# Performance work log

Hardware: AMD Instinct MI355X
Metric: run time of the kernel (lower is better)

## Reference

```python
import jax, jax.numpy as jnp
import numpy as np
import math

B, S, D, H = 1, 4096, 1024, 16
DH = D // H  # head_dim = 64
NEG = -10000.0  # matches torch masked-fill value in source (not -inf)


def setup_inputs() -> dict:
    key = jax.random.key(0)
    ks = jax.random.split(key, 5)
    scale = 0.02
    return {
        "x": jax.random.normal(ks[0], (B, S, D), dtype=jnp.float32),
        "Wqkv_w": jax.random.normal(ks[1], (3 * D, D), dtype=jnp.float32) * scale,
        "Wqkv_b": jax.random.normal(ks[2], (3 * D,), dtype=jnp.float32) * scale,
        "out_w": jax.random.normal(ks[3], (D, D), dtype=jnp.float32) * scale,
        "out_b": jax.random.normal(ks[4], (D,), dtype=jnp.float32) * scale,
    }


def reference(x, Wqkv_w, Wqkv_b, out_w, out_b):
    # QKV projection: (B,S,D) @ (D,3D) + b -> (B,S,3,H,DH)
    qkv = jnp.einsum('bsd,ed->bse', x, Wqkv_w) + Wqkv_b
    qkv = qkv.reshape(B, S, 3, H, DH)
    q, k, v = qkv[:, :, 0], qkv[:, :, 1], qkv[:, :, 2]  # each (B,S,H,DH)
    softmax_scale = 1.0 / math.sqrt(DH)
    # scores: (B,H,T,S)
    scores = jnp.einsum('bthd,bshd->bhts', q, k * softmax_scale)
    # causal additive mask with -10000 above diagonal (faithful to source)
    causal_mask = jnp.triu(jnp.full((S, S), NEG, dtype=scores.dtype), k=1)
    scores = scores + causal_mask
    attention = jax.nn.softmax(scores, axis=-1)
    context = jnp.einsum('bhts,bshd->bthd', attention, v)  # (B,T,H,DH)
    context = context.reshape(B, S, D)
    out = jnp.einsum('bsd,ed->bse', context, out_w) + out_b
    return out
```

## Files before the change

### kernel.cpp

```cpp
#include <hip/hip_runtime.h>
#include <hip/hip_bf16.h>

using f32x4  = __attribute__((ext_vector_type(4))) float;
using f32x16 = __attribute__((ext_vector_type(16))) float;
using bf16x8 = __attribute__((ext_vector_type(8))) __bf16;
using u16x8  = __attribute__((ext_vector_type(8))) unsigned short;
using u32x4  = __attribute__((ext_vector_type(4))) unsigned int;

#define DEV __device__ __forceinline__

constexpr int S_  = 4096;
constexpr int D_  = 1024;
constexpr int KD  = 1024;

constexpr size_t XB_OFF   = 0;
constexpr size_t WQKV_OFF = 8388608;
constexpr size_t WOUT_OFF = 14680064;
constexpr size_t QB_OFF   = 16777216;
constexpr size_t KB_OFF   = 25165824;
constexpr size_t VT_OFF   = 33554432;
constexpr size_t CTX_OFF  = 41943040;

DEV unsigned short f2bf(float f) {
  __hip_bfloat16 h = __float2bfloat16(f);
  return __builtin_bit_cast(unsigned short, h);
}

DEV void gl_lds16(const void* g, void* l) {
  __builtin_amdgcn_global_load_lds(
      (const __attribute__((address_space(1))) void*)g,
      (__attribute__((address_space(3))) void*)l, 16, 0, 0);
}

DEV f32x4 mfma16(bf16x8 a, bf16x8 b, f32x4 c) {
  return __builtin_amdgcn_mfma_f32_16x16x32_bf16(a, b, c, 0, 0, 0);
}
DEV f32x16 mfma32(bf16x8 a, bf16x8 b, f32x16 c) {
  return __builtin_amdgcn_mfma_f32_32x32x16_bf16(a, b, c, 0, 0, 0);
}
DEV unsigned cvtpk(float lo, float hi) {
  unsigned r;
  asm("v_cvt_pk_bf16_f32 %0, %1, %2" : "=v"(r) : "v"(lo), "v"(hi));
  return r;
}
DEV float exp2_fast(float x) {
  float r;
  asm("v_exp_f32 %0, %1" : "=v"(r) : "v"(x));
  return r;
}
DEV void pl32(unsigned& a, unsigned& b) {
  asm("v_permlane32_swap_b32 %0, %1" : "+v"(a), "+v"(b));
}
DEV float xhalf_add(float x) {
  float y;
  asm("v_mov_b32 %0, %1" : "=v"(y) : "v"(x));
  unsigned a = __builtin_bit_cast(unsigned, x), b = __builtin_bit_cast(unsigned, y);
  pl32(a, b);
  return __builtin_bit_cast(float, a) + __builtin_bit_cast(float, b);
}

__global__ void cvt_all_k(const float* __restrict__ x,
                          const float* __restrict__ wq,
                          const float* __restrict__ wo,
                          unsigned short* __restrict__ xb,
                          unsigned short* __restrict__ wqb,
                          unsigned short* __restrict__ wob) {
  for (int u = blockIdx.x * 256 + threadIdx.x; u < 1048576; u += 2048 * 256) {
    const float* s; unsigned short* d; int off;
    if (u < 524288)      { s = x;  d = xb;  off = u; }
    else if (u < 917504) { s = wq; d = wqb; off = u - 524288; }
    else                 { s = wo; d = wob; off = u - 917504; }
    const float4* s4 = (const float4*)s;
    float4 a = s4[2 * off], b = s4[2 * off + 1];
    u16x8 o;
    o[0] = f2bf(a.x); o[1] = f2bf(a.y); o[2] = f2bf(a.z); o[3] = f2bf(a.w);
    o[4] = f2bf(b.x); o[5] = f2bf(b.y); o[6] = f2bf(b.z); o[7] = f2bf(b.w);
    ((u16x8*)d)[off] = o;
  }
}

__global__ __launch_bounds__(256)
void gemm_qkv_k(const unsigned short* __restrict__ A,
                const unsigned short* __restrict__ Bt,
                const float* __restrict__ bias,
                unsigned short* __restrict__ qb,
                unsigned short* __restrict__ kb,
                unsigned short* __restrict__ vt) {
  __shared__ unsigned short As[2][4096];
  __shared__ unsigned short Bs[2][4096];
  const int t = threadIdx.x;
  const int w = t >> 6, l = t & 63;
  const int lr = l & 15, lg = l >> 4, lk = lg * 8;
  const int m0 = blockIdx.y * 128, n0 = blockIdx.x * 128;
  const int wm = (w >> 1) * 64, wn = (w & 1) * 64;

  f32x4 acc[4][4] = {};

  const int srow = t >> 2;
  const int scolb = (t & 3) << 4;
  const char* Ag = (const char*)A + (size_t)(m0 + srow) * (KD * 2) + scolb;
  const char* Bg = (const char*)Bt + (size_t)(n0 + srow) * (KD * 2) + scolb;

  auto stage = [&](int buf, int kt) {
    const char* ak = Ag + kt * 64;
    const char* bk = Bg + kt * 64;
    char* AsB = (char*)&As[buf][0];
    char* BsB = (char*)&Bs[buf][0];
    gl_lds16(ak,                 AsB + t * 16);
    gl_lds16(ak + 64 * (KD * 2), AsB + 4096 + t * 16);
    gl_lds16(bk,                 BsB + t * 16);
    gl_lds16(bk + 64 * (KD * 2), BsB + 4096 + t * 16);
  };

  stage(0, 0);
  for (int kt = 0; kt < KD / 32; ++kt) {
    __syncthreads();
    if (kt + 1 < KD / 32) stage((kt + 1) & 1, kt + 1);
    const int buf = kt & 1;

    bf16x8 a[4], b[4];
#pragma unroll
    for (int mi = 0; mi < 4; ++mi)
      a[mi] = *(const bf16x8*)&As[buf][(wm + mi * 16 + lr) * 32 + lk];
#pragma unroll
    for (int ni = 0; ni < 4; ++ni)
      b[ni] = *(const bf16x8*)&Bs[buf][(wn + ni * 16 + lr) * 32 + lk];
#pragma unroll
    for (int mi = 0; mi < 4; ++mi)
#pragma unroll
      for (int ni = 0; ni < 4; ++ni)
        acc[mi][ni] = mfma16(a[mi], b[ni], acc[mi][ni]);
  }

  const int r0 = lg * 4;
  const int which = n0 >> 10;
  const float kscale = 0.125f * 1.44269504088896f;
#pragma unroll
  for (int mi = 0; mi < 4; ++mi) {
    const int sbase = m0 + wm + mi * 16 + r0;
#pragma unroll
    for (int ni = 0; ni < 4; ++ni) {
      const int e = n0 + wn + ni * 16 + lr;
      const float bv = bias[e];
      const int h = (e & 1023) >> 6, dd = e & 63;
#pragma unroll
      for (int r = 0; r < 4; ++r) {
        const float v = acc[mi][ni][r] + bv;
        const int sr = sbase + r;
        if (which == 0)      qb[((size_t)(h * S_ + sr)) * 64 + dd] = f2bf(v);
        else if (which == 1) kb[((size_t)(h * S_ + sr)) * 64 + dd] = f2bf(v * kscale);
        else                 vt[((size_t)(h * 64 + dd)) * S_ + sr] = f2bf(v);
      }
    }
  }
}

__global__ __launch_bounds__(256)
void gemm_proj_k(const unsigned short* __restrict__ A,
                 const unsigned short* __restrict__ Bt,
                 const float* __restrict__ bias,
                 float* __restrict__ outf) {
  __shared__ unsigned short As[2][4096];
  __shared__ unsigned short Bs[2][2048];
  const int t = threadIdx.x;
  const int w = t >> 6, l = t & 63;
  const int lr = l & 15, lg = l >> 4, lk = lg * 8;
  const int m0 = blockIdx.y * 128, n0 = blockIdx.x * 64;
  const int wm = (w >> 1) * 64, wn = (w & 1) * 32;

  f32x4 acc[4][2] = {};

  const int srow = t >> 2;
  const int scolb = (t & 3) << 4;
  const char* Ag = (const char*)A + (size_t)(m0 + srow) * (KD * 2) + scolb;
  const char* Bg = (const char*)Bt + (size_t)(n0 + (t >> 2)) * (KD * 2) + scolb;

  auto stage = [&](int buf, int kt) {
    const char* ak = Ag + kt * 64;
    char* AsB = (char*)&As[buf][0];
    gl_lds16(ak,                 AsB + t * 16);
    gl_lds16(ak + 64 * (KD * 2), AsB + 4096 + t * 16);
    gl_lds16(Bg + kt * 64, (char*)&Bs[buf][0] + t * 16);
  };

  stage(0, 0);
  for (int kt = 0; kt < KD / 32; ++kt) {
    __syncthreads();
    if (kt + 1 < KD / 32) stage((kt + 1) & 1, kt + 1);
    const int buf = kt & 1;

    bf16x8 a[4], b[2];
#pragma unroll
    for (int mi = 0; mi < 4; ++mi)
      a[mi] = *(const bf16x8*)&As[buf][(wm + mi * 16 + lr) * 32 + lk];
#pragma unroll
    for (int ni = 0; ni < 2; ++ni)
      b[ni] = *(const bf16x8*)&Bs[buf][(wn + ni * 16 + lr) * 32 + lk];
#pragma unroll
    for (int mi = 0; mi < 4; ++mi)
#pragma unroll
      for (int ni = 0; ni < 2; ++ni)
        acc[mi][ni] = mfma16(a[mi], b[ni], acc[mi][ni]);
  }

  const int r0 = lg * 4;
#pragma unroll
  for (int mi = 0; mi < 4; ++mi) {
    const int sbase = m0 + wm + mi * 16 + r0;
#pragma unroll
    for (int ni = 0; ni < 2; ++ni) {
      const int e = n0 + wn + ni * 16 + lr;
      const float bv = bias[e];
#pragma unroll
      for (int r = 0; r < 4; ++r)
        outf[(size_t)(sbase + r) * D_ + e] = acc[mi][ni][r] + bv;
    }
  }
}

__global__ __launch_bounds__(512, 2)
void attn_k(const unsigned short* __restrict__ Qb,
            const unsigned short* __restrict__ Kb,
            const unsigned short* __restrict__ Vt,
            unsigned short* __restrict__ ctx) {
  __shared__ char smem[65536];

  const int t = threadIdx.x;
  const int w8 = t >> 6;
  const int g  = w8 >> 2;
  const int w  = w8 & 3;
  const int l = t & 63, lq = l & 31, hi = l >> 5;
  const int b = blockIdx.x + (blockIdx.y << 4);
  const int h = ((b & 7) << 1) | ((b >> 3) & 1);
  const int pairIdx = b >> 4;

  const int sg = t >> 8;
  const int ts = t & 255;
  const int srow = ts >> 3;
  const int ssw  = ((ts & 7) << 4) ^ ((srow & 7) << 4);
  const char* Kg0 = (const char*)Kb + (size_t)(h * S_) * 128;
  const char* Vg0 = (const char*)Vt + (size_t)(h * 64) * (size_t)(S_ * 2);

  for (int task = 0; task < 2; ++task) {
    const int bi = task == 0 ? (31 - pairIdx) : pairIdx;
    const int q0 = bi * 128;
    const int qrow = q0 + w * 32 + lq;
    const int qwmin = q0 + w * 32, qwmax = qwmin + 31;
    const int niter = bi + 1;

    const unsigned short* Qr = Qb + ((size_t)(h * S_ + qrow)) * 64;
    bf16x8 qf[4];
#pragma unroll
    for (int d0 = 0; d0 < 4; ++d0)
      qf[d0] = *(const bf16x8*)(Qr + d0 * 16 + hi * 8);

    f32x16 cacc[2] = {};
    float lsum = 0.f;

    auto stage = [&](int buf, int tl) {
      const int kv0 = tl * 64;
      char* kd = smem + sg * 16384 + buf * 8192;
      const char* Kg = Kg0 + (size_t)kv0 * 128;
      gl_lds16(Kg + (size_t)srow * 128 + ssw,        kd + ts * 16);
      gl_lds16(Kg + (size_t)(32 + srow) * 128 + ssw, kd + 4096 + ts * 16);
      char* vd = smem + 32768 + sg * 16384 + buf * 8192;
      const char* Vg = Vg0 + (size_t)kv0 * 2;
      gl_lds16(Vg + (size_t)srow * (S_ * 2) + ssw,        vd + ts * 16);
      gl_lds16(Vg + (size_t)(32 + srow) * (S_ * 2) + ssw, vd + 4096 + ts * 16);
    };

    int cur = 0;
    stage(0, sg * niter);

    for (int it = 0; it < niter; ++it) {
      __syncthreads();
      if (it + 1 < niter) stage(cur ^ 1, it + 1 + sg * niter);
      const char* Kt = smem + g * 16384 + cur * 8192;
      const char* Vl = smem + 32768 + g * 16384 + cur * 8192;
      const int tl = it + g * niter;

      if (tl * 64 + 63 <= qwmin) {
        f32x16 st0, st1;
#pragma unroll
        for (int r = 0; r < 16; ++r) { st0[r] = -8.0f; st1[r] = -8.0f; }
        const char* kb0 = Kt + lq * 128;
        const char* kb1 = Kt + (32 + lq) * 128;
        const int ksw = (lq & 7) << 4;
        __builtin_amdgcn_s_setprio(1);
#pragma unroll
        for (int d0 = 0; d0 < 4; ++d0) {
          bf16x8 kf0 = *(const bf16x8*)(kb0 + ((d0 * 32 + hi * 16) ^ ksw));
          bf16x8 kf1 = *(const bf16x8*)(kb1 + ((d0 * 32 + hi * 16) ^ ksw));
          st0 = mfma32(kf0, qf[d0], st0);
          st1 = mfma32(kf1, qf[d0], st1);
        }
        __builtin_amdgcn_s_setprio(0);

#pragma unroll
        for (int r = 0; r < 16; ++r) { st0[r] = exp2_fast(st0[r]); st1[r] = exp2_fast(st1[r]); }
        float a0 = (st0[0] + st0[1]) + (st0[2] + st0[3]);
        float a1 = (st0[4] + st0[5]) + (st0[6] + st0[7]);
        float a2 = (st0[8] + st0[9]) + (st0[10] + st0[11]);
        float a3 = (st0[12] + st0[13]) + (st0[14] + st0[15]);
        float b0 = (st1[0] + st1[1]) + (st1[2] + st1[3]);
        float b1 = (st1[4] + st1[5]) + (st1[6] + st1[7]);
        float b2 = (st1[8] + st1[9]) + (st1[10] + st1[11]);
        float b3 = (st1[12] + st1[13]) + (st1[14] + st1[15]);
        lsum += xhalf_add(((a0 + a1) + (a2 + a3)) + ((b0 + b1) + (b2 + b3)));

        unsigned x0 = cvtpk(st0[0], st0[1]),   x1 = cvtpk(st0[2], st0[3]);
        unsigned y0 = cvtpk(st0[4], st0[5]),   y1 = cvtpk(st0[6], st0[7]);
        pl32(x0, y0); pl32(x1, y1);
        u32x4 f00 = {x0, x1, y0, y1};
        bf16x8 pf00 = __builtin_bit_cast(bf16x8, f00);
        unsigned x2 = cvtpk(st0[8], st0[9]),   x3 = cvtpk(st0[10], st0[11]);
        unsigned y2 = cvtpk(st0[12], st0[13]), y3 = cvtpk(st0[14], st0[15]);
        pl32(x2, y2); pl32(x3, y3);
        u32x4 f01 = {x2, x3, y2, y3};
        bf16x8 pf01 = __builtin_bit_cast(bf16x8, f01);
        unsigned u0 = cvtpk(st1[0], st1[1]),   u1 = cvtpk(st1[2], st1[3]);
        unsigned v0w = cvtpk(st1[4], st1[5]),  v1w = cvtpk(st1[6], st1[7]);
        pl32(u0, v0w); pl32(u1, v1w);
        u32x4 f10 = {u0, u1, v0w, v1w};
        bf16x8 pf10 = __builtin_bit_cast(bf16x8, f10);
        unsigned u2 = cvtpk(st1[8], st1[9]),   u3 = cvtpk(st1[10], st1[11]);
        unsigned v2w = cvtpk(st1[12], st1[13]), v3w = cvtpk(st1[14], st1[15]);
        pl32(u2, v2w); pl32(u3, v3w);
        u32x4 f11 = {u2, u3, v2w, v3w};
        bf16x8 pf11 = __builtin_bit_cast(bf16x8, f11);

        __builtin_amdgcn_s_setprio(1);
#pragma unroll
        for (int db = 0; db < 2; ++db) {
          const int dr = db * 32 + lq;
          const char* vbase = Vl + dr * 128;
          const int vsw = (dr & 7) << 4;
          bf16x8 va = *(const bf16x8*)(vbase + ((hi * 16) ^ vsw));
          bf16x8 vb = *(const bf16x8*)(vbase + ((32 + hi * 16) ^ vsw));
          bf16x8 vc = *(const bf16x8*)(vbase + ((64 + hi * 16) ^ vsw));
          bf16x8 vd = *(const bf16x8*)(vbase + ((96 + hi * 16) ^ vsw));
          cacc[db] = mfma32(va, pf00, cacc[db]);
          cacc[db] = mfma32(vb, pf01, cacc[db]);
          cacc[db] = mfma32(vc, pf10, cacc[db]);
          cacc[db] = mfma32(vd, pf11, cacc[db]);
        }
        __builtin_amdgcn_s_setprio(0);
      } else {
#pragma unroll
        for (int kvh = 0; kvh < 2; ++kvh) {
          const int kv0s = tl * 64 + kvh * 32;
          if (kv0s > qwmax) continue;

          f32x16 st;
#pragma unroll
          for (int r = 0; r < 16; ++r) st[r] = -8.0f;
          const int kr = kvh * 32 + lq;
          const char* kbase = Kt + kr * 128;
          const int ksw = (kr & 7) << 4;
#pragma unroll
          for (int d0 = 0; d0 < 4; ++d0) {
            bf16x8 kf = *(const bf16x8*)(kbase + ((d0 * 32 + hi * 16) ^ ksw));
            st = mfma32(kf, qf[d0], st);
          }

          if (kv0s + 31 > qwmin) {
#pragma unroll
            for (int r = 0; r < 16; ++r) {
              const int kvg = kv0s + (r & 3) + 8 * (r >> 2) + 4 * hi;
              if (kvg > qrow) st[r] = -INFINITY;
            }
          }

#pragma unroll
          for (int r = 0; r < 16; ++r) st[r] = exp2_fast(st[r]);
          float a0 = (st[0] + st[1]) + (st[2] + st[3]);
          float a1 = (st[4] + st[5]) + (st[6] + st[7]);
          float a2 = (st[8] + st[9]) + (st[10] + st[11]);
          float a3 = (st[12] + st[13]) + (st[14] + st[15]);
          lsum += xhalf_add((a0 + a1) + (a2 + a3));

          unsigned x0 = cvtpk(st[0], st[1]),   x1 = cvtpk(st[2], st[3]);
          unsigned y0 = cvtpk(st[4], st[5]),   y1 = cvtpk(st[6], st[7]);
          pl32(x0, y0); pl32(x1, y1);
          u32x4 f0 = {x0, x1, y0, y1};
          bf16x8 pf0 = __builtin_bit_cast(bf16x8, f0);
          unsigned x2 = cvtpk(st[8], st[9]),   x3 = cvtpk(st[10], st[11]);
          unsigned y2 = cvtpk(st[12], st[13]), y3 = cvtpk(st[14], st[15]);
          pl32(x2, y2); pl32(x3, y3);
          u32x4 f1 = {x2, x3, y2, y3};
          bf16x8 pf1 = __builtin_bit_cast(bf16x8, f1);

#pragma unroll
          for (int db = 0; db < 2; ++db) {
            const int dr = db * 32 + lq;
            const char* vbase = Vl + dr * 128;
            const int vsw = (dr & 7) << 4;
            bf16x8 v0 = *(const bf16x8*)(vbase + ((kvh * 64 + hi * 16) ^ vsw));
            bf16x8 v1 = *(const bf16x8*)(vbase + ((kvh * 64 + 32 + hi * 16) ^ vsw));
            cacc[db] = mfma32(v0, pf0, cacc[db]);
            cacc[db] = mfma32(v1, pf1, cacc[db]);
          }
        }
      }
      cur ^= 1;
    }

    __syncthreads();
    float* slot = (float*)smem + (size_t)(w * 64 + l) * 36;
    if (g == 1) {
      slot[0] = lsum;
#pragma unroll
      for (int j = 0; j < 16; ++j) { slot[1 + j] = cacc[0][j]; slot[17 + j] = cacc[1][j]; }
    }
    __syncthreads();
    if (g == 0) {
      const float inv = 1.0f / (lsum + slot[0]);
      unsigned short* base = ctx + (size_t)qrow * D_ + h * 64;
#pragma unroll
      for (int db = 0; db < 2; ++db)
#pragma unroll
        for (int r = 0; r < 16; r += 2) {
          const float o0 = (cacc[db][r]     + slot[1 + db * 16 + r])     * inv;
          const float o1 = (cacc[db][r + 1] + slot[1 + db * 16 + r + 1]) * inv;
          const unsigned wv = cvtpk(o0, o1);
          const int d = (r & 3) + 8 * (r >> 2) + 4 * hi + 32 * db;
          *(unsigned*)(base + d) = wv;
        }
    }
    __syncthreads();
  }
}

extern "C" void kernel_launch(void* const* d_in, const int* in_sizes, int n_in,
                              void* d_out, int out_size, void* d_ws, size_t ws_size,
                              hipStream_t stream) {
  const float* x      = (const float*)d_in[0];
  const float* Wqkv_w = (const float*)d_in[1];
  const float* Wqkv_b = (const float*)d_in[2];
  const float* out_w  = (const float*)d_in[3];
  const float* out_b  = (const float*)d_in[4];
  float* out = (float*)d_out;
  char* ws = (char*)d_ws;

  unsigned short* xb    = (unsigned short*)(ws + XB_OFF);
  unsigned short* wqkvb = (unsigned short*)(ws + WQKV_OFF);
  unsigned short* woutb = (unsigned short*)(ws + WOUT_OFF);
  unsigned short* Qb    = (unsigned short*)(ws + QB_OFF);
  unsigned short* Kb    = (unsigned short*)(ws + KB_OFF);
  unsigned short* Vt    = (unsigned short*)(ws + VT_OFF);
  unsigned short* ctx   = (unsigned short*)(ws + CTX_OFF);

  cvt_all_k<<<2048, 256, 0, stream>>>(x, Wqkv_w, out_w, xb, wqkvb, woutb);

  gemm_qkv_k<<<dim3(24, 32), 256, 0, stream>>>(xb, wqkvb, Wqkv_b, Qb, Kb, Vt);

  attn_k<<<dim3(16, 16), 512, 0, stream>>>(Qb, Kb, Vt, ctx);

  gemm_proj_k<<<dim3(16, 32), 256, 0, stream>>>(ctx, woutb, out_b, out);
}
```

Measured before the change: 131.4 us.

## Process 128-row KV tiles per iteration in the causal attention kernel

Doubles the K/V tile staged in LDS per loop iteration from 64 to 128 keys. This halves the number of iterations and block barriers per query tile. The KV range is now split between the two wave groups as contiguous halves rather than interleaved tiles. The V layout moves to 256-byte rows with a new swizzle. Shared memory doubles to 128 KB per block, which likely stops two 512-thread blocks from fitting on a CU and lowers occupancy.

```diff
diff --git a/kernel.cpp b/kernel.cpp
--- a/kernel.cpp
+++ b/kernel.cpp
@@ -223,7 +223,7 @@
             const unsigned short* __restrict__ Kb,
             const unsigned short* __restrict__ Vt,
             unsigned short* __restrict__ ctx) {
-  __shared__ char smem[65536];
+  __shared__ char smem[131072];
 
   const int t = threadIdx.x;
   const int w8 = t >> 6;
@@ -236,8 +236,10 @@
 
   const int sg = t >> 8;
   const int ts = t & 255;
-  const int srow = ts >> 3;
-  const int ssw  = ((ts & 7) << 4) ^ ((srow & 7) << 4);
+  const int srow  = ts >> 3;
+  const int ssw   = ((ts & 7) << 4) ^ ((srow & 7) << 4);
+  const int srowV = ts >> 4;
+  const int ssv   = ((ts & 15) << 4) ^ ((srowV & 7) << 4);
   const char* Kg0 = (const char*)Kb + (size_t)(h * S_) * 128;
   const char* Vg0 = (const char*)Vt + (size_t)(h * 64) * (size_t)(S_ * 2);
 
@@ -246,7 +248,10 @@
     const int q0 = bi * 128;
     const int qrow = q0 + w * 32 + lq;
     const int qwmin = q0 + w * 32, qwmax = qwmin + 31;
-    const int niter = bi + 1;
+    const int niter  = (bi + 2) >> 1;
+    const int sgbase = sg == 0 ? 0 : (bi + 1) * 64;
+    const int gbase  = g  == 0 ? 0 : (bi + 1) * 64;
+    const int kvend  = g == 0 ? (bi + 1) * 64 : S_;
 
     const unsigned short* Qr = Qb + ((size_t)(h * S_ + qrow)) * 64;
     bf16x8 qf[4];
@@ -257,106 +262,110 @@
     f32x16 cacc[2] = {};
     float lsum = 0.f;
 
-    auto stage = [&](int buf, int tl) {
-      const int kv0 = tl * 64;
-      char* kd = smem + sg * 16384 + buf * 8192;
+    auto stage = [&](int buf, int tt) {
+      const int kv0 = sgbase + tt * 128;
+      char* kd = smem + sg * 32768 + buf * 16384;
       const char* Kg = Kg0 + (size_t)kv0 * 128;
-      gl_lds16(Kg + (size_t)srow * 128 + ssw,        kd + ts * 16);
-      gl_lds16(Kg + (size_t)(32 + srow) * 128 + ssw, kd + 4096 + ts * 16);
-      char* vd = smem + 32768 + sg * 16384 + buf * 8192;
+#pragma unroll
+      for (int c = 0; c < 4; ++c)
+        gl_lds16(Kg + (size_t)(srow + c * 32) * 128 + ssw, kd + c * 4096 + ts * 16);
+      char* vd = smem + 65536 + sg * 32768 + buf * 16384;
       const char* Vg = Vg0 + (size_t)kv0 * 2;
-      gl_lds16(Vg + (size_t)srow * (S_ * 2) + ssw,        vd + ts * 16);
-      gl_lds16(Vg + (size_t)(32 + srow) * (S_ * 2) + ssw, vd + 4096 + ts * 16);
+#pragma unroll
+      for (int c = 0; c < 4; ++c)
+        gl_lds16(Vg + (size_t)(srowV + c * 16) * (S_ * 2) + ssv, vd + c * 4096 + ts * 16);
     };
 
     int cur = 0;
-    stage(0, sg * niter);
+    stage(0, 0);
 
     for (int it = 0; it < niter; ++it) {
       __syncthreads();
-      if (it + 1 < niter) stage(cur ^ 1, it + 1 + sg * niter);
-      const char* Kt = smem + g * 16384 + cur * 8192;
-      const char* Vl = smem + 32768 + g * 16384 + cur * 8192;
-      const int tl = it + g * niter;
-
-      if (tl * 64 + 63 <= qwmin) {
-        f32x16 st0, st1;
-#pragma unroll
-        for (int r = 0; r < 16; ++r) { st0[r] = -8.0f; st1[r] = -8.0f; }
-        const char* kb0 = Kt + lq * 128;
-        const char* kb1 = Kt + (32 + lq) * 128;
-        const int ksw = (lq & 7) << 4;
-        __builtin_amdgcn_s_setprio(1);
-#pragma unroll
-        for (int d0 = 0; d0 < 4; ++d0) {
-          bf16x8 kf0 = *(const bf16x8*)(kb0 + ((d0 * 32 + hi * 16) ^ ksw));
-          bf16x8 kf1 = *(const bf16x8*)(kb1 + ((d0 * 32 + hi * 16) ^ ksw));
-          st0 = mfma32(kf0, qf[d0], st0);
-          st1 = mfma32(kf1, qf[d0], st1);
+      if (it + 1 < niter) stage(cur ^ 1, it + 1);
+      const char* Kt = smem + g * 32768 + cur * 16384;
+      const char* Vl = smem + 65536 + g * 32768 + cur * 16384;
+      const int tk0 = gbase + it * 128;
+
+      if (tk0 + 127 <= qwmin && tk0 + 128 <= kvend) {
+#pragma unroll
+        for (int hf = 0; hf < 2; ++hf) {
+          f32x16 st0, st1;
+#pragma unroll
+          for (int r = 0; r < 16; ++r) { st0[r] = -8.0f; st1[r] = -8.0f; }
+          const char* kb0 = Kt + (hf * 64 + lq) * 128;
+          const char* kb1 = Kt + (hf * 64 + 32 + lq) * 128;
+          const int ksw = (lq & 7) << 4;
+          __builtin_amdgcn_s_setprio(1);
+#pragma unroll
+          for (int d0 = 0; d0 < 4; ++d0) {
+            bf16x8 kf0 = *(const bf16x8*)(kb0 + ((d0 * 32 + hi * 16) ^ ksw));
+            bf16x8 kf1 = *(const bf16x8*)(kb1 + ((d0 * 32 + hi * 16) ^ ksw));
+            st0 = mfma32(kf0, qf[d0], st0);
+            st1 = mfma32(kf1, qf[d0], st1);
+          }
+          __builtin_amdgcn_s_setprio(0);
+
+#pragma unroll
+          for (int r = 0; r < 16; ++r) { st0[r] = exp2_fast(st0[r]); st1[r] = exp2_fast(st1[r]); }
+          float a0 = (st0[0] + st0[1]) + (st0[2] + st0[3]);
+          float a1 = (st0[4] + st0[5]) + (st0[6] + st0[7]);
+          float a2 = (st0[8] + st0[9]) + (st0[10] + st0[11]);
+          float a3 = (st0[12] + st0[13]) + (st0[14] + st0[15]);
+          float b0 = (st1[0] + st1[1]) + (st1[2] + st1[3]);
+          float b1 = (st1[4] + st1[5]) + (st1[6] + st1[7]);
+          float b2 = (st1[8] + st1[9]) + (st1[10] + st1[11]);
+          float b3 = (st1[12] + st1[13]) + (st1[14] + st1[15]);
+          lsum += xhalf_add(((a0 + a1) + (a2 + a3)) + ((b0 + b1) + (b2 + b3)));
+
+          unsigned x0 = cvtpk(st0[0], st0[1]),   x1 = cvtpk(st0[2], st0[3]);
+          unsigned y0 = cvtpk(st0[4], st0[5]),   y1 = cvtpk(st0[6], st0[7]);
+          pl32(x0, y0); pl32(x1, y1);
+          u32x4 f00 = {x0, x1, y0, y1};
+          bf16x8 pf00 = __builtin_bit_cast(bf16x8, f00);
+          unsigned x2 = cvtpk(st0[8], st0[9]),   x3 = cvtpk(st0[10], st0[11]);
+          unsigned y2 = cvtpk(st0[12], st0[13]), y3 = cvtpk(st0[14], st0[15]);
+          pl32(x2, y2); pl32(x3, y3);
+          u32x4 f01 = {x2, x3, y2, y3};
+          bf16x8 pf01 = __builtin_bit_cast(bf16x8, f01);
+          unsigned u0 = cvtpk(st1[0], st1[1]),    u1 = cvtpk(st1[2], st1[3]);
+          unsigned v0w = cvtpk(st1[4], st1[5]),   v1w = cvtpk(st1[6], st1[7]);
+          pl32(u0, v0w); pl32(u1, v1w);
+          u32x4 f10 = {u0, u1, v0w, v1w};
+          bf16x8 pf10 = __builtin_bit_cast(bf16x8, f10);
+          unsigned u2 = cvtpk(st1[8], st1[9]),    u3 = cvtpk(st1[10], st1[11]);
+          unsigned v2w = cvtpk(st1[12], st1[13]), v3w = cvtpk(st1[14], st1[15]);
+          pl32(u2, v2w); pl32(u3, v3w);
+          u32x4 f11 = {u2, u3, v2w, v3w};
+          bf16x8 pf11 = __builtin_bit_cast(bf16x8, f11);
+
+          __builtin_amdgcn_s_setprio(1);
+#pragma unroll
+          for (int db = 0; db < 2; ++db) {
+            const int dr = db * 32 + lq;
+            const char* vbase = Vl + dr * 256;
+            const int vsw = (dr & 7) << 4;
+            bf16x8 va = *(const bf16x8*)(vbase + ((hf * 128 + hi * 16) ^ vsw));
+            bf16x8 vb = *(const bf16x8*)(vbase + ((hf * 128 + 32 + hi * 16) ^ vsw));
+            bf16x8 vc = *(const bf16x8*)(vbase + ((hf * 128 + 64 + hi * 16) ^ vsw));
+            bf16x8 vd = *(const bf16x8*)(vbase + ((hf * 128 + 96 + hi * 16) ^ vsw));
+            cacc[db] = mfma32(va, pf00, cacc[db]);
+            cacc[db] = mfma32(vb, pf01, cacc[db]);
+            cacc[db] = mfma32(vc, pf10, cacc[db]);
+            cacc[db] = mfma32(vd, pf11, cacc[db]);
+          }
+          __builtin_amdgcn_s_setprio(0);
         }
-        __builtin_amdgcn_s_setprio(0);
-
-#pragma unroll
-        for (int r = 0; r < 16; ++r) { st0[r] = exp2_fast(st0[r]); st1[r] = exp2_fast(st1[r]); }
-        float a0 = (st0[0] + st0[1]) + (st0[2] + st0[3]);
-        float a1 = (st0[4] + st0[5]) + (st0[6] + st0[7]);
-        float a2 = (st0[8] + st0[9]) + (st0[10] + st0[11]);
-        float a3 = (st0[12] + st0[13]) + (st0[14] + st0[15]);
-        float b0 = (st1[0] + st1[1]) + (st1[2] + st1[3]);
-        float b1 = (st1[4] + st1[5]) + (st1[6] + st1[7]);
-        float b2 = (st1[8] + st1[9]) + (st1[10] + st1[11]);
-        float b3 = (st1[12] + st1[13]) + (st1[14] + st1[15]);
-        lsum += xhalf_add(((a0 + a1) + (a2 + a3)) + ((b0 + b1) + (b2 + b3)));
-
-        unsigned x0 = cvtpk(st0[0], st0[1]),   x1 = cvtpk(st0[2], st0[3]);
-        unsigned y0 = cvtpk(st0[4], st0[5]),   y1 = cvtpk(st0[6], st0[7]);
-        pl32(x0, y0); pl32(x1, y1);
-        u32x4 f00 = {x0, x1, y0, y1};
-        bf16x8 pf00 = __builtin_bit_cast(bf16x8, f00);
-        unsigned x2 = cvtpk(st0[8], st0[9]),   x3 = cvtpk(st0[10], st0[11]);
-        unsigned y2 = cvtpk(st0[12], st0[13]), y3 = cvtpk(st0[14], st0[15]);
-        pl32(x2, y2); pl32(x3, y3);
-        u32x4 f01 = {x2, x3, y2, y3};
-        bf16x8 pf01 = __builtin_bit_cast(bf16x8, f01);
-        unsigned u0 = cvtpk(st1[0], st1[1]),   u1 = cvtpk(st1[2], st1[3]);
-        unsigned v0w = cvtpk(st1[4], st1[5]),  v1w = cvtpk(st1[6], st1[7]);
-        pl32(u0, v0w); pl32(u1, v1w);
-        u32x4 f10 = {u0, u1, v0w, v1w};
-        bf16x8 pf10 = __builtin_bit_cast(bf16x8, f10);
-        unsigned u2 = cvtpk(st1[8], st1[9]),   u3 = cvtpk(st1[10], st1[11]);
-        unsigned v2w = cvtpk(st1[12], st1[13]), v3w = cvtpk(st1[14], st1[15]);
-        pl32(u2, v2w); pl32(u3, v3w);
-        u32x4 f11 = {u2, u3, v2w, v3w};
-        bf16x8 pf11 = __builtin_bit_cast(bf16x8, f11);
-
-        __builtin_amdgcn_s_setprio(1);
-#pragma unroll
-        for (int db = 0; db < 2; ++db) {
-          const int dr = db * 32 + lq;
-          const char* vbase = Vl + dr * 128;
-          const int vsw = (dr & 7) << 4;
-          bf16x8 va = *(const bf16x8*)(vbase + ((hi * 16) ^ vsw));
-          bf16x8 vb = *(const bf16x8*)(vbase + ((32 + hi * 16) ^ vsw));
-          bf16x8 vc = *(const bf16x8*)(vbase + ((64 + hi * 16) ^ vsw));
-          bf16x8 vd = *(const bf16x8*)(vbase + ((96 + hi * 16) ^ vsw));
-          cacc[db] = mfma32(va, pf00, cacc[db]);
-          cacc[db] = mfma32(vb, pf01, cacc[db]);
-          cacc[db] = mfma32(vc, pf10, cacc[db]);
-          cacc[db] = mfma32(vd, pf11, cacc[db]);
-        }
-        __builtin_amdgcn_s_setprio(0);
       } else {
 #pragma unroll
-        for (int kvh = 0; kvh < 2; ++kvh) {
-          const int kv0s = tl * 64 + kvh * 32;
-          if (kv0s > qwmax) continue;
+        for (int s = 0; s < 4; ++s) {
+          const int kv0s = tk0 + s * 32;
+          if (kv0s >= kvend || kv0s > qwmax) continue;
 
           f32x16 st;
 #pragma unroll
           for (int r = 0; r < 16; ++r) st[r] = -8.0f;
-          const int kr = kvh * 32 + lq;
-          const char* kbase = Kt + kr * 128;
-          const int ksw = (kr & 7) << 4;
+          const char* kbase = Kt + (s * 32 + lq) * 128;
+          const int ksw = (lq & 7) << 4;
 #pragma unroll
           for (int d0 = 0; d0 < 4; ++d0) {
             bf16x8 kf = *(const bf16x8*)(kbase + ((d0 * 32 + hi * 16) ^ ksw));
@@ -393,10 +402,10 @@
 #pragma unroll
           for (int db = 0; db < 2; ++db) {
             const int dr = db * 32 + lq;
-            const char* vbase = Vl + dr * 128;
+            const char* vbase = Vl + dr * 256;
             const int vsw = (dr & 7) << 4;
-            bf16x8 v0 = *(const bf16x8*)(vbase + ((kvh * 64 + hi * 16) ^ vsw));
-            bf16x8 v1 = *(const bf16x8*)(vbase + ((kvh * 64 + 32 + hi * 16) ^ vsw));
+            bf16x8 v0 = *(const bf16x8*)(vbase + ((s * 64 + hi * 16) ^ vsw));
+            bf16x8 v1 = *(const bf16x8*)(vbase + ((s * 64 + 32 + hi * 16) ^ vsw));
             cacc[db] = mfma32(v0, pf0, cacc[db]);
             cacc[db] = mfma32(v1, pf1, cacc[db]);
           }
```

Measured after the change: 130.4 us. Within noise of the previous version (-0.8%).

## Halve attention query tile to 64 rows, using 256-thread blocks and twice the blocks

Applied to the files above, without the earlier changes.

The causal attention kernel now processes 64 query rows per block with 4 waves instead of 128 rows with 8 waves, and launches twice as many blocks. The KV tiles of a query block are split between two wave groups, with a guard for an odd tile count. Each thread now issues four async loads per staged K and V tile instead of two. The aim is finer load balancing and more scheduling freedom across CUs, at the cost of streaming K and V from global memory twice as often per query row.

```diff
diff --git a/kernel.cpp b/kernel.cpp
--- a/kernel.cpp
+++ b/kernel.cpp
@@ -218,7 +218,7 @@
   }
 }
 
-__global__ __launch_bounds__(512, 2)
+__global__ __launch_bounds__(256, 2)
 void attn_k(const unsigned short* __restrict__ Qb,
             const unsigned short* __restrict__ Kb,
             const unsigned short* __restrict__ Vt,
@@ -226,27 +226,29 @@
   __shared__ char smem[65536];
 
   const int t = threadIdx.x;
-  const int w8 = t >> 6;
-  const int g  = w8 >> 2;
-  const int w  = w8 & 3;
+  const int w4 = t >> 6;
+  const int g  = w4 >> 1;
+  const int w  = w4 & 1;
   const int l = t & 63, lq = l & 31, hi = l >> 5;
-  const int b = blockIdx.x + (blockIdx.y << 4);
+  const int b = blockIdx.x + (blockIdx.y << 5);
   const int h = ((b & 7) << 1) | ((b >> 3) & 1);
   const int pairIdx = b >> 4;
 
-  const int sg = t >> 8;
-  const int ts = t & 255;
+  const int sg = t >> 7;
+  const int ts = t & 127;
   const int srow = ts >> 3;
   const int ssw  = ((ts & 7) << 4) ^ ((srow & 7) << 4);
   const char* Kg0 = (const char*)Kb + (size_t)(h * S_) * 128;
   const char* Vg0 = (const char*)Vt + (size_t)(h * 64) * (size_t)(S_ * 2);
 
   for (int task = 0; task < 2; ++task) {
-    const int bi = task == 0 ? (31 - pairIdx) : pairIdx;
-    const int q0 = bi * 128;
+    const int bi = task == 0 ? (63 - pairIdx) : pairIdx;
+    const int q0 = bi * 64;
     const int qrow = q0 + w * 32 + lq;
     const int qwmin = q0 + w * 32, qwmax = qwmin + 31;
-    const int niter = bi + 1;
+    const int ntiles = bi + 1;
+    const int niter  = (ntiles + 1) >> 1;
+    const int mycnt  = sg == 0 ? niter : (ntiles - niter);
 
     const unsigned short* Qr = Qb + ((size_t)(h * S_ + qrow)) * 64;
     bf16x8 qf[4];
@@ -257,148 +259,152 @@
     f32x16 cacc[2] = {};
     float lsum = 0.f;
 
-    auto stage = [&](int buf, int tl) {
-      const int kv0 = tl * 64;
+    auto stage = [&](int buf, int idx) {
+      const int kv0 = ((sg ? niter : 0) + idx) * 64;
       char* kd = smem + sg * 16384 + buf * 8192;
       const char* Kg = Kg0 + (size_t)kv0 * 128;
-      gl_lds16(Kg + (size_t)srow * 128 + ssw,        kd + ts * 16);
-      gl_lds16(Kg + (size_t)(32 + srow) * 128 + ssw, kd + 4096 + ts * 16);
+#pragma unroll
+      for (int c = 0; c < 4; ++c)
+        gl_lds16(Kg + (size_t)(srow + c * 16) * 128 + ssw, kd + c * 2048 + ts * 16);
       char* vd = smem + 32768 + sg * 16384 + buf * 8192;
       const char* Vg = Vg0 + (size_t)kv0 * 2;
-      gl_lds16(Vg + (size_t)srow * (S_ * 2) + ssw,        vd + ts * 16);
-      gl_lds16(Vg + (size_t)(32 + srow) * (S_ * 2) + ssw, vd + 4096 + ts * 16);
+#pragma unroll
+      for (int c = 0; c < 4; ++c)
+        gl_lds16(Vg + (size_t)(srow + c * 16) * (S_ * 2) + ssw, vd + c * 2048 + ts * 16);
     };
 
     int cur = 0;
-    stage(0, sg * niter);
+    if (mycnt > 0) stage(0, 0);
 
     for (int it = 0; it < niter; ++it) {
       __syncthreads();
-      if (it + 1 < niter) stage(cur ^ 1, it + 1 + sg * niter);
-      const char* Kt = smem + g * 16384 + cur * 8192;
-      const char* Vl = smem + 32768 + g * 16384 + cur * 8192;
-      const int tl = it + g * niter;
-
-      if (tl * 64 + 63 <= qwmin) {
-        f32x16 st0, st1;
-#pragma unroll
-        for (int r = 0; r < 16; ++r) { st0[r] = -8.0f; st1[r] = -8.0f; }
-        const char* kb0 = Kt + lq * 128;
-        const char* kb1 = Kt + (32 + lq) * 128;
-        const int ksw = (lq & 7) << 4;
-        __builtin_amdgcn_s_setprio(1);
-#pragma unroll
-        for (int d0 = 0; d0 < 4; ++d0) {
-          bf16x8 kf0 = *(const bf16x8*)(kb0 + ((d0 * 32 + hi * 16) ^ ksw));
-          bf16x8 kf1 = *(const bf16x8*)(kb1 + ((d0 * 32 + hi * 16) ^ ksw));
-          st0 = mfma32(kf0, qf[d0], st0);
-          st1 = mfma32(kf1, qf[d0], st1);
-        }
-        __builtin_amdgcn_s_setprio(0);
-
-#pragma unroll
-        for (int r = 0; r < 16; ++r) { st0[r] = exp2_fast(st0[r]); st1[r] = exp2_fast(st1[r]); }
-        float a0 = (st0[0] + st0[1]) + (st0[2] + st0[3]);
-        float a1 = (st0[4] + st0[5]) + (st0[6] + st0[7]);
-        float a2 = (st0[8] + st0[9]) + (st0[10] + st0[11]);
-        float a3 = (st0[12] + st0[13]) + (st0[14] + st0[15]);
-        float b0 = (st1[0] + st1[1]) + (st1[2] + st1[3]);
-        float b1 = (st1[4] + st1[5]) + (st1[6] + st1[7]);
-        float b2 = (st1[8] + st1[9]) + (st1[10] + st1[11]);
-        float b3 = (st1[12] + st1[13]) + (st1[14] + st1[15]);
-        lsum += xhalf_add(((a0 + a1) + (a2 + a3)) + ((b0 + b1) + (b2 + b3)));
-
-        unsigned x0 = cvtpk(st0[0], st0[1]),   x1 = cvtpk(st0[2], st0[3]);
-        unsigned y0 = cvtpk(st0[4], st0[5]),   y1 = cvtpk(st0[6], st0[7]);
-        pl32(x0, y0); pl32(x1, y1);
-        u32x4 f00 = {x0, x1, y0, y1};
-        bf16x8 pf00 = __builtin_bit_cast(bf16x8, f00);
-        unsigned x2 = cvtpk(st0[8], st0[9]),   x3 = cvtpk(st0[10], st0[11]);
-        unsigned y2 = cvtpk(st0[12], st0[13]), y3 = cvtpk(st0[14], st0[15]);
-        pl32(x2, y2); pl32(x3, y3);
-        u32x4 f01 = {x2, x3, y2, y3};
-        bf16x8 pf01 = __builtin_bit_cast(bf16x8, f01);
-        unsigned u0 = cvtpk(st1[0], st1[1]),   u1 = cvtpk(st1[2], st1[3]);
-        unsigned v0w = cvtpk(st1[4], st1[5]),  v1w = cvtpk(st1[6], st1[7]);
-        pl32(u0, v0w); pl32(u1, v1w);
-        u32x4 f10 = {u0, u1, v0w, v1w};
-        bf16x8 pf10 = __builtin_bit_cast(bf16x8, f10);
-        unsigned u2 = cvtpk(st1[8], st1[9]),   u3 = cvtpk(st1[10], st1[11]);
-        unsigned v2w = cvtpk(st1[12], st1[13]), v3w = cvtpk(st1[14], st1[15]);
-        pl32(u2, v2w); pl32(u3, v3w);
-        u32x4 f11 = {u2, u3, v2w, v3w};
-        bf16x8 pf11 = __builtin_bit_cast(bf16x8, f11);
-
-        __builtin_amdgcn_s_setprio(1);
-#pragma unroll
-        for (int db = 0; db < 2; ++db) {
-          const int dr = db * 32 + lq;
-          const char* vbase = Vl + dr * 128;
-          const int vsw = (dr & 7) << 4;
-          bf16x8 va = *(const bf16x8*)(vbase + ((hi * 16) ^ vsw));
-          bf16x8 vb = *(const bf16x8*)(vbase + ((32 + hi * 16) ^ vsw));
-          bf16x8 vc = *(const bf16x8*)(vbase + ((64 + hi * 16) ^ vsw));
-          bf16x8 vd = *(const bf16x8*)(vbase + ((96 + hi * 16) ^ vsw));
-          cacc[db] = mfma32(va, pf00, cacc[db]);
-          cacc[db] = mfma32(vb, pf01, cacc[db]);
-          cacc[db] = mfma32(vc, pf10, cacc[db]);
-          cacc[db] = mfma32(vd, pf11, cacc[db]);
-        }
-        __builtin_amdgcn_s_setprio(0);
-      } else {
-#pragma unroll
-        for (int kvh = 0; kvh < 2; ++kvh) {
-          const int kv0s = tl * 64 + kvh * 32;
-          if (kv0s > qwmax) continue;
-
-          f32x16 st;
-#pragma unroll
-          for (int r = 0; r < 16; ++r) st[r] = -8.0f;
-          const int kr = kvh * 32 + lq;
-          const char* kbase = Kt + kr * 128;
-          const int ksw = (kr & 7) << 4;
+      if (it + 1 < mycnt) stage(cur ^ 1, it + 1);
+      const int tl = (g ? niter : 0) + it;
+      if (tl < ntiles) {
+        const char* Kt = smem + g * 16384 + cur * 8192;
+        const char* Vl = smem + 32768 + g * 16384 + cur * 8192;
+
+        if (tl * 64 + 63 <= qwmin) {
+          f32x16 st0, st1;
+#pragma unroll
+          for (int r = 0; r < 16; ++r) { st0[r] = -8.0f; st1[r] = -8.0f; }
+          const char* kb0 = Kt + lq * 128;
+          const char* kb1 = Kt + (32 + lq) * 128;
+          const int ksw = (lq & 7) << 4;
+          __builtin_amdgcn_s_setprio(1);
 #pragma unroll
           for (int d0 = 0; d0 < 4; ++d0) {
-            bf16x8 kf = *(const bf16x8*)(kbase + ((d0 * 32 + hi * 16) ^ ksw));
-            st = mfma32(kf, qf[d0], st);
+            bf16x8 kf0 = *(const bf16x8*)(kb0 + ((d0 * 32 + hi * 16) ^ ksw));
+            bf16x8 kf1 = *(const bf16x8*)(kb1 + ((d0 * 32 + hi * 16) ^ ksw));
+            st0 = mfma32(kf0, qf[d0], st0);
+            st1 = mfma32(kf1, qf[d0], st1);
           }
-
-          if (kv0s + 31 > qwmin) {
-#pragma unroll
-            for (int r = 0; r < 16; ++r) {
-              const int kvg = kv0s + (r & 3) + 8 * (r >> 2) + 4 * hi;
-              if (kvg > qrow) st[r] = -INFINITY;
-            }
-          }
-
-#pragma unroll
-          for (int r = 0; r < 16; ++r) st[r] = exp2_fast(st[r]);
-          float a0 = (st[0] + st[1]) + (st[2] + st[3]);
-          float a1 = (st[4] + st[5]) + (st[6] + st[7]);
-          float a2 = (st[8] + st[9]) + (st[10] + st[11]);
-          float a3 = (st[12] + st[13]) + (st[14] + st[15]);
-          lsum += xhalf_add((a0 + a1) + (a2 + a3));
-
-          unsigned x0 = cvtpk(st[0], st[1]),   x1 = cvtpk(st[2], st[3]);
-          unsigned y0 = cvtpk(st[4], st[5]),   y1 = cvtpk(st[6], st[7]);
+          __builtin_amdgcn_s_setprio(0);
+
+#pragma unroll
+          for (int r = 0; r < 16; ++r) { st0[r] = exp2_fast(st0[r]); st1[r] = exp2_fast(st1[r]); }
+          float a0 = (st0[0] + st0[1]) + (st0[2] + st0[3]);
+          float a1 = (st0[4] + st0[5]) + (st0[6] + st0[7]);
+          float a2 = (st0[8] + st0[9]) + (st0[10] + st0[11]);
+          float a3 = (st0[12] + st0[13]) + (st0[14] + st0[15]);
+          float b0 = (st1[0] + st1[1]) + (st1[2] + st1[3]);
+          float b1 = (st1[4] + st1[5]) + (st1[6] + st1[7]);
+          float b2 = (st1[8] + st1[9]) + (st1[10] + st1[11]);
+          float b3 = (st1[12] + st1[13]) + (st1[14] + st1[15]);
+          lsum += xhalf_add(((a0 + a1) + (a2 + a3)) + ((b0 + b1) + (b2 + b3)));
+
+          unsigned x0 = cvtpk(st0[0], st0[1]),   x1 = cvtpk(st0[2], st0[3]);
+          unsigned y0 = cvtpk(st0[4], st0[5]),   y1 = cvtpk(st0[6], st0[7]);
           pl32(x0, y0); pl32(x1, y1);
-          u32x4 f0 = {x0, x1, y0, y1};
-          bf16x8 pf0 = __builtin_bit_cast(bf16x8, f0);
-          unsigned x2 = cvtpk(st[8], st[9]),   x3 = cvtpk(st[10], st[11]);
-          unsigned y2 = cvtpk(st[12], st[13]), y3 = cvtpk(st[14], st[15]);
+          u32x4 f00 = {x0, x1, y0, y1};
+          bf16x8 pf00 = __builtin_bit_cast(bf16x8, f00);
+          unsigned x2 = cvtpk(st0[8], st0[9]),   x3 = cvtpk(st0[10], st0[11]);
+          unsigned y2 = cvtpk(st0[12], st0[13]), y3 = cvtpk(st0[14], st0[15]);
           pl32(x2, y2); pl32(x3, y3);
-          u32x4 f1 = {x2, x3, y2, y3};
-          bf16x8 pf1 = __builtin_bit_cast(bf16x8, f1);
-
+          u32x4 f01 = {x2, x3, y2, y3};
+          bf16x8 pf01 = __builtin_bit_cast(bf16x8, f01);
+          unsigned u0 = cvtpk(st1[0], st1[1]),    u1 = cvtpk(st1[2], st1[3]);
+          unsigned v0w = cvtpk(st1[4], st1[5]),   v1w = cvtpk(st1[6], st1[7]);
+          pl32(u0, v0w); pl32(u1, v1w);
+          u32x4 f10 = {u0, u1, v0w, v1w};
+          bf16x8 pf10 = __builtin_bit_cast(bf16x8, f10);
+          unsigned u2 = cvtpk(st1[8], st1[9]),    u3 = cvtpk(st1[10], st1[11]);
+          unsigned v2w = cvtpk(st1[12], st1[13]), v3w = cvtpk(st1[14], st1[15]);
+          pl32(u2, v2w); pl32(u3, v3w);
+          u32x4 f11 = {u2, u3, v2w, v3w};
+          bf16x8 pf11 = __builtin_bit_cast(bf16x8, f11);
+
+          __builtin_amdgcn_s_setprio(1);
 #pragma unroll
           for (int db = 0; db < 2; ++db) {
             const int dr = db * 32 + lq;
             const char* vbase = Vl + dr * 128;
             const int vsw = (dr & 7) << 4;
-            bf16x8 v0 = *(const bf16x8*)(vbase + ((kvh * 64 + hi * 16) ^ vsw));
-            bf16x8 v1 = *(const bf16x8*)(vbase + ((kvh * 64 + 32 + hi * 16) ^ vsw));
-            cacc[db] = mfma32(v0, pf0, cacc[db]);
-            cacc[db] = mfma32(v1, pf1, cacc[db]);
+            bf16x8 va = *(const bf16x8*)(vbase + ((hi * 16) ^ vsw));
+            bf16x8 vb = *(const bf16x8*)(vbase + ((32 + hi * 16) ^ vsw));
+            bf16x8 vc = *(const bf16x8*)(vbase + ((64 + hi * 16) ^ vsw));
+            bf16x8 vd = *(const bf16x8*)(vbase + ((96 + hi * 16) ^ vsw));
+            cacc[db] = mfma32(va, pf00, cacc[db]);
+            cacc[db] = mfma32(vb, pf01, cacc[db]);
+            cacc[db] = mfma32(vc, pf10, cacc[db]);
+            cacc[db] = mfma32(vd, pf11, cacc[db]);
+          }
+          __builtin_amdgcn_s_setprio(0);
+        } else {
+#pragma unroll
+          for (int kvh = 0; kvh < 2; ++kvh) {
+            const int kv0s = tl * 64 + kvh * 32;
+            if (kv0s > qwmax) continue;
+
+            f32x16 st;
+#pragma unroll
+            for (int r = 0; r < 16; ++r) st[r] = -8.0f;
+            const int kr = kvh * 32 + lq;
+            const char* kbase = Kt + kr * 128;
+            const int ksw = (kr & 7) << 4;
+#pragma unroll
+            for (int d0 = 0; d0 < 4; ++d0) {
+              bf16x8 kf = *(const bf16x8*)(kbase + ((d0 * 32 + hi * 16) ^ ksw));
+              st = mfma32(kf, qf[d0], st);
+            }
+
+            if (kv0s + 31 > qwmin) {
+#pragma unroll
+              for (int r = 0; r < 16; ++r) {
+                const int kvg = kv0s + (r & 3) + 8 * (r >> 2) + 4 * hi;
+                if (kvg > qrow) st[r] = -INFINITY;
+              }
+            }
+
+#pragma unroll
+            for (int r = 0; r < 16; ++r) st[r] = exp2_fast(st[r]);
+            float a0 = (st[0] + st[1]) + (st[2] + st[3]);
+            float a1 = (st[4] + st[5]) + (st[6] + st[7]);
+            float a2 = (st[8] + st[9]) + (st[10] + st[11]);
+            float a3 = (st[12] + st[13]) + (st[14] + st[15]);
+            lsum += xhalf_add((a0 + a1) + (a2 + a3));
+
+            unsigned x0 = cvtpk(st[0], st[1]),   x1 = cvtpk(st[2], st[3]);
+            unsigned y0 = cvtpk(st[4], st[5]),   y1 = cvtpk(st[6], st[7]);
+            pl32(x0, y0); pl32(x1, y1);
+            u32x4 f0 = {x0, x1, y0, y1};
+            bf16x8 pf0 = __builtin_bit_cast(bf16x8, f0);
+            unsigned x2 = cvtpk(st[8], st[9]),   x3 = cvtpk(st[10], st[11]);
+            unsigned y2 = cvtpk(st[12], st[13]), y3 = cvtpk(st[14], st[15]);
+            pl32(x2, y2); pl32(x3, y3);
+            u32x4 f1 = {x2, x3, y2, y3};
+            bf16x8 pf1 = __builtin_bit_cast(bf16x8, f1);
+
+#pragma unroll
+            for (int db = 0; db < 2; ++db) {
+              const int dr = db * 32 + lq;
+              const char* vbase = Vl + dr * 128;
+              const int vsw = (dr & 7) << 4;
+              bf16x8 v0 = *(const bf16x8*)(vbase + ((kvh * 64 + hi * 16) ^ vsw));
+              bf16x8 v1 = *(const bf16x8*)(vbase + ((kvh * 64 + 32 + hi * 16) ^ vsw));
+              cacc[db] = mfma32(v0, pf0, cacc[db]);
+              cacc[db] = mfma32(v1, pf1, cacc[db]);
+            }
           }
         }
       }
@@ -454,7 +460,7 @@
 
   gemm_qkv_k<<<dim3(24, 32), 256, 0, stream>>>(xb, wqkvb, Wqkv_b, Qb, Kb, Vt);
 
-  attn_k<<<dim3(16, 16), 512, 0, stream>>>(Qb, Kb, Vt, ctx);
+  attn_k<<<dim3(32, 16), 256, 0, stream>>>(Qb, Kb, Vt, ctx);
 
   gemm_proj_k<<<dim3(16, 32), 256, 0, stream>>>(ctx, woutb, out_b, out);
 }
```

Result: slower. 135.5 us (+3.1%).
